# Kernel optimization log

Hardware: AMD Instinct MI355X
Metric: run time of the kernel (lower is better)

Reference implementation:

```python
import jax, jax.numpy as jnp
import numpy as np

B, L, D = 2, 2048, 2560
H, KV, HD = 8, 4, 256
FF = 10240
WINDOW = 1024
ROPE_BASE = 10000.0
EPS = 1e-6


def rmsnorm(x, scale=None):
    x32 = x.astype(jnp.float32)
    var = jnp.mean(jnp.square(x32), axis=-1, keepdims=True)
    xn = x32 * jax.lax.rsqrt(var + EPS)
    return xn if scale is None else xn * scale.astype(jnp.float32)


def apply_rope(x, positions, base):
    # full RoPE (rope_fraction=1.0): rotate pairs (i, i+head_dim//2)
    hd = x.shape[-1]
    half = hd // 2
    timescale = base ** (2.0 * jnp.arange(half, dtype=jnp.float32) / hd)
    ang = positions[:, :, None].astype(jnp.float32) / timescale  # [B,L,half]
    sin = jnp.sin(ang)[:, :, None, :]  # [B,L,1,half]
    cos = jnp.cos(ang)[:, :, None, :]
    x1, x2 = x[..., :half], x[..., half:]
    return jnp.concatenate([x1 * cos - x2 * sin, x2 * cos + x1 * sin], axis=-1)


def setup_inputs() -> dict:
    key = jax.random.key(0)
    ks = jax.random.split(key, 16)
    s = lambda fan_in: 1.0 / np.sqrt(fan_in)
    return {
        "x": jax.random.normal(ks[0], (B, L, D), jnp.float32),
        "positions": jnp.broadcast_to(jnp.arange(L, dtype=jnp.int32), (B, L)),
        "wq": jax.random.normal(ks[1], (D, H * HD), jnp.float32) * s(D),
        "wk": jax.random.normal(ks[2], (D, KV * HD), jnp.float32) * s(D),
        "wv": jax.random.normal(ks[3], (D, KV * HD), jnp.float32) * s(D),
        "wo": jax.random.normal(ks[4], (H * HD, D), jnp.float32) * s(H * HD),
        "q_scale": jnp.ones((HD,), jnp.float32),
        "k_scale": jnp.ones((HD,), jnp.float32),
        "pre_attn_scale": jnp.ones((D,), jnp.float32),
        "post_attn_scale": jnp.ones((D,), jnp.float32),
        "pre_ffw_scale": jnp.ones((D,), jnp.float32),
        "post_ffw_scale": jnp.ones((D,), jnp.float32),
        "w_gate": jax.random.normal(ks[5], (D, FF), jnp.float32) * s(D),
        "w_up": jax.random.normal(ks[6], (D, FF), jnp.float32) * s(D),
        "w_down": jax.random.normal(ks[7], (FF, D), jnp.float32) * s(FF),
    }


def reference(x, positions, wq, wk, wv, wo, q_scale, k_scale,
              pre_attn_scale, post_attn_scale, pre_ffw_scale, post_ffw_scale,
              w_gate, w_up, w_down):
    # --- attention sub-block ---
    h = rmsnorm(x, pre_attn_scale)
    q = (h @ wq).reshape(B, L, H, HD)
    k = (h @ wk).reshape(B, L, KV, HD)
    v = (h @ wv).reshape(B, L, KV, HD)
    q = apply_rope(rmsnorm(q, q_scale), positions, ROPE_BASE)
    k = apply_rope(rmsnorm(k, k_scale), positions, ROPE_BASE)
    v = rmsnorm(v)  # RMSNormNoScale on V
    rep = H // KV
    k = jnp.repeat(k, rep, axis=2)  # [B,L,H,HD]
    v = jnp.repeat(v, rep, axis=2)
    scores = jnp.einsum("bqhd,bkhd->bhqk", q, k)  # NOTE: no 1/sqrt(d) scaling, faithful to source
    i = jnp.arange(L)[:, None]
    j = jnp.arange(L)[None, :]
    mask = (j <= i) & (j > i - WINDOW)  # causal & sliding window
    scores = jnp.where(mask[None, None, :, :], scores, -10000.0)
    probs = jax.nn.softmax(scores.astype(jnp.float32), axis=-1)
    attn = jnp.einsum("bhqk,bkhd->bqhd", probs, v).reshape(B, L, H * HD)
    attn = attn @ wo
    x = x + rmsnorm(attn, post_attn_scale)
    # --- feedforward sub-block (GeGLU) ---
    h = rmsnorm(x, pre_ffw_scale)
    hidden = jax.nn.gelu(h @ w_gate, approximate=False) * (h @ w_up)
    ffw = hidden @ w_down
    x = x + rmsnorm(ffw, post_ffw_scale)
    return x
```

## Files before the change

kernel.cpp:

```cpp
#include <hip/hip_runtime.h>
#include <math.h>

#define DEV __device__ __forceinline__

typedef _Float16 f16;
typedef _Float16 f16x8 __attribute__((ext_vector_type(8)));
typedef _Float16 f16x4 __attribute__((ext_vector_type(4)));
typedef float f32x4 __attribute__((ext_vector_type(4)));

DEV void gload_lds16(const void* g, void* l) {
  __builtin_amdgcn_global_load_lds(
      (const __attribute__((address_space(1))) void*)g,
      (__attribute__((address_space(3))) void*)l, 16, 0, 0);
}

__global__ void transpose_w(const float* __restrict__ src, f16* __restrict__ dst,
                            int R, int C) {
  __shared__ float tile[32][33];
  int c0 = blockIdx.x * 32, r0 = blockIdx.y * 32;
  int tx = threadIdx.x, ty = threadIdx.y;
#pragma unroll
  for (int j = 0; j < 32; j += 8)
    tile[ty + j][tx] = src[(size_t)(r0 + ty + j) * C + c0 + tx];
  __syncthreads();
#pragma unroll
  for (int j = 0; j < 32; j += 8)
    dst[(size_t)(c0 + ty + j) * R + r0 + tx] = (f16)tile[tx][ty + j];
}

__global__ void rope_table_k(float* __restrict__ tab) {
  int idx = blockIdx.x * 256 + threadIdx.x;
  int pos = idx >> 7, j = idx & 127;
  float ts = powf(10000.0f, (float)j * (1.0f / 128.0f));
  float ang = (float)pos / ts;
  tab[pos * 256 + j] = sinf(ang);
  tab[pos * 256 + 128 + j] = cosf(ang);
}

__global__ __launch_bounds__(256) void rmsnorm_f32_f16(
    const float* __restrict__ in, const float* __restrict__ scale,
    f16* __restrict__ out) {
  constexpr int D = 2560, N4 = D / 4;
  const int m = blockIdx.x, tid = threadIdx.x;
  const float* row = in + (size_t)m * D;
  float vals[12];
  float ss = 0.f;
#pragma unroll
  for (int it = 0; it < 3; ++it) {
    int c4 = tid + it * 256;
    if (c4 < N4) {
      float4 v = *(const float4*)(row + c4 * 4);
      vals[it * 4 + 0] = v.x; vals[it * 4 + 1] = v.y;
      vals[it * 4 + 2] = v.z; vals[it * 4 + 3] = v.w;
      ss += v.x * v.x + v.y * v.y + v.z * v.z + v.w * v.w;
    }
  }
#pragma unroll
  for (int off = 32; off; off >>= 1) ss += __shfl_xor(ss, off, 64);
  __shared__ float red[4];
  if ((tid & 63) == 0) red[tid >> 6] = ss;
  __syncthreads();
  float rs = rsqrtf((red[0] + red[1] + red[2] + red[3]) * (1.0f / D) + 1e-6f);
#pragma unroll
  for (int it = 0; it < 3; ++it) {
    int c4 = tid + it * 256;
    if (c4 < N4) {
      float4 sc = *(const float4*)(scale + c4 * 4);
      f16x4 o;
      o[0] = (f16)(vals[it * 4 + 0] * rs * sc.x);
      o[1] = (f16)(vals[it * 4 + 1] * rs * sc.y);
      o[2] = (f16)(vals[it * 4 + 2] * rs * sc.z);
      o[3] = (f16)(vals[it * 4 + 3] * rs * sc.w);
      *(f16x4*)(out + (size_t)m * D + c4 * 4) = o;
    }
  }
}

__global__ __launch_bounds__(256) void residual_rmsnorm(
    const float* x, const f16* __restrict__ y,
    const float* __restrict__ scale, float* out) {
  constexpr int D = 2560, N4 = D / 4;
  const int m = blockIdx.x, tid = threadIdx.x;
  const f16* yr = y + (size_t)m * D;
  float yv[12];
  float ss = 0.f;
#pragma unroll
  for (int it = 0; it < 3; ++it) {
    int c4 = tid + it * 256;
    if (c4 < N4) {
      f16x4 u = *(const f16x4*)(yr + c4 * 4);
      float a = (float)u[0], b = (float)u[1], c = (float)u[2], d = (float)u[3];
      yv[it * 4 + 0] = a; yv[it * 4 + 1] = b; yv[it * 4 + 2] = c; yv[it * 4 + 3] = d;
      ss += a * a + b * b + c * c + d * d;
    }
  }
#pragma unroll
  for (int off = 32; off; off >>= 1) ss += __shfl_xor(ss, off, 64);
  __shared__ float red[4];
  if ((tid & 63) == 0) red[tid >> 6] = ss;
  __syncthreads();
  float rs = rsqrtf((red[0] + red[1] + red[2] + red[3]) * (1.0f / D) + 1e-6f);
#pragma unroll
  for (int it = 0; it < 3; ++it) {
    int c4 = tid + it * 256;
    if (c4 < N4) {
      float4 xv = *(const float4*)(x + (size_t)m * D + c4 * 4);
      float4 sc = *(const float4*)(scale + c4 * 4);
      float4 o;
      o.x = xv.x + yv[it * 4 + 0] * rs * sc.x;
      o.y = xv.y + yv[it * 4 + 1] * rs * sc.y;
      o.z = xv.z + yv[it * 4 + 2] * rs * sc.z;
      o.w = xv.w + yv[it * 4 + 3] * rs * sc.w;
      *(float4*)(out + (size_t)m * D + c4 * 4) = o;
    }
  }
}

__global__ __launch_bounds__(256) void norm_rope_k(
    const f16* __restrict__ qkv, const int* __restrict__ positions,
    const float* __restrict__ q_scale, const float* __restrict__ k_scale,
    const float* __restrict__ tab,
    f16* __restrict__ q_g, f16* __restrict__ k_g, f16* __restrict__ v_n) {
  const int m = blockIdx.x;
  const int tid = threadIdx.x, w = tid >> 6, l = tid & 63;
  const int pos = positions[m];
  const float* srow = tab + (size_t)pos * 256;
  const int c0 = l * 4;
  for (int vi = w; vi < 16; vi += 4) {
    f16x4 u = *(const f16x4*)(qkv + (size_t)m * 4096 + vi * 256 + c0);
    float x0 = (float)u[0], x1 = (float)u[1], x2 = (float)u[2], x3 = (float)u[3];
    float ss = x0 * x0 + x1 * x1 + x2 * x2 + x3 * x3;
#pragma unroll
    for (int off = 32; off; off >>= 1) ss += __shfl_xor(ss, off, 64);
    float rs = rsqrtf(ss * (1.0f / 256.0f) + 1e-6f);
    if (vi < 12) {
      const float* sc = (vi < 8) ? q_scale : k_scale;
      float4 s4 = *(const float4*)(sc + c0);
      float n0 = x0 * rs * s4.x, n1 = x1 * rs * s4.y;
      float n2 = x2 * rs * s4.z, n3 = x3 * rs * s4.w;
      float p0 = __shfl_xor(n0, 32, 64), p1 = __shfl_xor(n1, 32, 64);
      float p2 = __shfl_xor(n2, 32, 64), p3 = __shfl_xor(n3, 32, 64);
      int j0 = c0 & 127;
      float4 sn = *(const float4*)(srow + j0);
      float4 cs = *(const float4*)(srow + 128 + j0);
      float sgn = (l < 32) ? -1.0f : 1.0f;
      f16x4 o;
      o[0] = (f16)(n0 * cs.x + sgn * p0 * sn.x);
      o[1] = (f16)(n1 * cs.y + sgn * p1 * sn.y);
      o[2] = (f16)(n2 * cs.z + sgn * p2 * sn.z);
      o[3] = (f16)(n3 * cs.w + sgn * p3 * sn.w);
      if (vi < 8) *(f16x4*)(q_g + (size_t)m * 2048 + vi * 256 + c0) = o;
      else        *(f16x4*)(k_g + (size_t)m * 1024 + (vi - 8) * 256 + c0) = o;
    } else {
      f16x4 o;
      o[0] = (f16)(x0 * rs); o[1] = (f16)(x1 * rs);
      o[2] = (f16)(x2 * rs); o[3] = (f16)(x3 * rs);
      *(f16x4*)(v_n + (size_t)m * 1024 + (vi - 12) * 256 + c0) = o;
    }
  }
}

__global__ void transpose_v_k(const f16* __restrict__ v_n, f16* __restrict__ vt) {
  __shared__ f16 tile[32][33];
  int bkv = blockIdx.z;
  int b = bkv >> 2, kv = bkv & 3;
  int t0 = blockIdx.x * 32, d0 = blockIdx.y * 32;
  int tx = threadIdx.x, ty = threadIdx.y;
#pragma unroll
  for (int j = 0; j < 32; j += 8)
    tile[ty + j][tx] =
        v_n[(size_t)(b * 2048 + t0 + ty + j) * 1024 + kv * 256 + d0 + tx];
  __syncthreads();
#pragma unroll
  for (int j = 0; j < 32; j += 8)
    vt[((size_t)bkv * 256 + d0 + ty + j) * 2048 + t0 + tx] = tile[tx][ty + j];
}

template <int EPI>
__global__ __launch_bounds__(512, 2) void gemm256(
    const f16* __restrict__ A, const f16* __restrict__ BT,
    f16* __restrict__ C, const f16* __restrict__ aux, int M, int N, int K) {
  extern __shared__ __align__(16) f16 lds[];
  const int tid = threadIdx.x;
  const int w = tid >> 6, l = tid & 63;
  const int l15 = l & 15, lk = l >> 4;
  const int wm = w >> 2, wn = w & 3;

  const int gx = gridDim.x;
  const int nwg = gx * gridDim.y;
  const int orig = blockIdx.y * gx + blockIdx.x;
  const int swz = (orig & 7) * (nwg >> 3) + (orig >> 3);
  const int bn = swz % gx, bm = swz / gx;

  const f16* Ab = A + (size_t)bm * 256 * K;
  const f16* Bb = BT + (size_t)bn * 256 * K;
  const int NT = K >> 6;

  const int srow = tid >> 2;
  const int sg = (tid & 3) ^ ((srow >> 1) & 3);
  const f16* srcA = Ab + (size_t)srow * K + sg * 8;
  const f16* srcB = Bb + (size_t)srow * K + sg * 8;

  auto stage = [&](int op, int kh, int buf, int kt) {
    const f16* src = (op ? srcB : srcA) + kt * 64 + kh * 32;
    f16* dst = lds + ((buf << 2) + (kh << 1) + op) * 8192 + tid * 8;
    gload_lds16(src, dst);
    gload_lds16(src + (size_t)128 * K, dst + 4096);
  };

  const int fcol = (lk ^ ((l15 >> 1) & 3)) << 3;
  const int aoff = (wm * 128 + l15) * 32 + fcol;
  const int boff = 8192 + (wn * 64 + l15) * 32 + fcol;

  f32x4 acc[8][4] = {};

  stage(0, 0, 0, 0);
  stage(1, 0, 0, 0);
  stage(0, 1, 0, 0);
  stage(1, 1, 0, 0);
  if (NT > 1) stage(0, 0, 1, 1);
  asm volatile("s_waitcnt vmcnt(6)" ::: "memory");
  __builtin_amdgcn_s_barrier();
  asm volatile("" ::: "memory");

  for (int t = 0; t < NT; ++t) {
    const int buf = t & 1, nbuf = buf ^ 1;
    const f16* lb0 = lds + buf * 32768;
    const f16* lb1 = lb0 + 16384;
    {
      f16x8 a1[4], b[4], a2[4];
#pragma unroll
      for (int i = 0; i < 4; ++i) a1[i] = *(const f16x8*)(lb0 + aoff + i * 512);
#pragma unroll
      for (int i = 0; i < 4; ++i) b[i] = *(const f16x8*)(lb0 + boff + i * 512);
#pragma unroll
      for (int i = 0; i < 4; ++i) a2[i] = *(const f16x8*)(lb0 + aoff + (4 + i) * 512);
      if (t + 1 < NT) stage(1, 0, nbuf, t + 1);
      __builtin_amdgcn_s_setprio(1);
#pragma unroll
      for (int mi = 0; mi < 4; ++mi)
#pragma unroll
        for (int ni = 0; ni < 4; ++ni)
          acc[mi][ni] = __builtin_amdgcn_mfma_f32_16x16x32_f16(a1[mi], b[ni], acc[mi][ni], 0, 0, 0);
      __builtin_amdgcn_s_setprio(0);
      if (t + 1 < NT) stage(0, 1, nbuf, t + 1);
      __builtin_amdgcn_s_setprio(1);
#pragma unroll
      for (int mi = 0; mi < 4; ++mi)
#pragma unroll
        for (int ni = 0; ni < 4; ++ni)
          acc[4 + mi][ni] = __builtin_amdgcn_mfma_f32_16x16x32_f16(a2[mi], b[ni], acc[4 + mi][ni], 0, 0, 0);
      __builtin_amdgcn_s_setprio(0);
    }
    if (t + 1 < NT) asm volatile("s_waitcnt vmcnt(6)" ::: "memory");
    else            asm volatile("s_waitcnt vmcnt(0)" ::: "memory");
    __builtin_amdgcn_s_barrier();
    asm volatile("" ::: "memory");
    {
      f16x8 a1[4], b[4], a2[4];
#pragma unroll
      for (int i = 0; i < 4; ++i) a1[i] = *(const f16x8*)(lb1 + aoff + i * 512);
#pragma unroll
      for (int i = 0; i < 4; ++i) b[i] = *(const f16x8*)(lb1 + boff + i * 512);
#pragma unroll
      for (int i = 0; i < 4; ++i) a2[i] = *(const f16x8*)(lb1 + aoff + (4 + i) * 512);
      if (t + 1 < NT) stage(1, 1, nbuf, t + 1);
      __builtin_amdgcn_s_setprio(1);
#pragma unroll
      for (int mi = 0; mi < 4; ++mi)
#pragma unroll
        for (int ni = 0; ni < 4; ++ni)
          acc[mi][ni] = __builtin_amdgcn_mfma_f32_16x16x32_f16(a1[mi], b[ni], acc[mi][ni], 0, 0, 0);
      __builtin_amdgcn_s_setprio(0);
      if (t + 2 < NT) stage(0, 0, buf, t + 2);
      __builtin_amdgcn_s_setprio(1);
#pragma unroll
      for (int mi = 0; mi < 4; ++mi)
#pragma unroll
        for (int ni = 0; ni < 4; ++ni)
          acc[4 + mi][ni] = __builtin_amdgcn_mfma_f32_16x16x32_f16(a2[mi], b[ni], acc[4 + mi][ni], 0, 0, 0);
      __builtin_amdgcn_s_setprio(0);
    }
    if (t + 2 < NT)      asm volatile("s_waitcnt vmcnt(6)" ::: "memory");
    else if (t + 1 < NT) asm volatile("s_waitcnt vmcnt(4)" ::: "memory");
    else                 asm volatile("s_waitcnt vmcnt(0)" ::: "memory");
    __builtin_amdgcn_s_barrier();
    asm volatile("" ::: "memory");
  }

#pragma unroll
  for (int mi = 0; mi < 8; ++mi) {
#pragma unroll
    for (int ni = 0; ni < 4; ++ni) {
#pragma unroll
      for (int i = 0; i < 4; ++i) {
        int row = bm * 256 + wm * 128 + mi * 16 + lk * 4 + i;
        int col = bn * 256 + wn * 64 + ni * 16 + l15;
        size_t idx = (size_t)row * N + col;
        float v = acc[mi][ni][i];
        if constexpr (EPI == 1) {
          v = 0.5f * v * (1.0f + erff(v * 0.70710678118654752f));
        } else if constexpr (EPI == 2) {
          v *= (float)aux[idx];
        }
        C[idx] = (f16)v;
      }
    }
  }
}

__global__ __launch_bounds__(256) void flash_attn_k(
    const f16* __restrict__ q_g, const f16* __restrict__ k_g,
    const f16* __restrict__ vt, f16* __restrict__ ctx) {
  constexpr int KP = 264, VP = 40, PP = 40;
  __shared__ f16 Ks[32 * KP];
  __shared__ f16 Vs[256 * VP];
  __shared__ f16 Ps[4][16 * PP];
  const int qt = blockIdx.x, h = blockIdx.y, b = blockIdx.z;
  const int tid = threadIdx.x, w = tid >> 6, l = tid & 63;
  const int l15 = l & 15, lk = l >> 4;
  const int kv = h >> 1;

  f16x8 aq[8];
  const int qrow = qt * 64 + w * 16 + l15;
  const f16* qp = q_g + (size_t)(b * 2048 + qrow) * 2048 + h * 256 + lk * 8;
#pragma unroll
  for (int kc = 0; kc < 8; ++kc) aq[kc] = *(const f16x8*)(qp + kc * 32);

  f32x4 o[16] = {};
  float mrow[4] = {-1e30f, -1e30f, -1e30f, -1e30f};
  float lrow[4] = {0.f, 0.f, 0.f, 0.f};

  int kt_lo = 2 * qt - 32; if (kt_lo < 0) kt_lo = 0;
  const int kt_hi = 2 * qt + 1;
  const int iqb = qt * 64 + w * 16 + lk * 4;

  for (int kt = kt_lo; kt <= kt_hi; ++kt) {
    __syncthreads();
#pragma unroll
    for (int it = 0; it < 4; ++it) {
      int ch = tid + it * 256;
      int jl = ch >> 5, kcc = (ch & 31) * 8;
      *(f16x8*)&Ks[jl * KP + kcc] = *(const f16x8*)(
          k_g + (size_t)(b * 2048 + kt * 32 + jl) * 1024 + kv * 256 + kcc);
      int d = ch >> 2, tc = (ch & 3) * 8;
      *(f16x8*)&Vs[d * VP + tc] = *(const f16x8*)(
          vt + ((size_t)(b * 4 + kv) * 256 + d) * 2048 + kt * 32 + tc);
    }
    __syncthreads();
    f32x4 s[2] = {};
#pragma unroll
    for (int ct = 0; ct < 2; ++ct)
#pragma unroll
      for (int kc = 0; kc < 8; ++kc) {
        f16x8 bk = *(const f16x8*)&Ks[(ct * 16 + l15) * KP + kc * 32 + lk * 8];
        s[ct] = __builtin_amdgcn_mfma_f32_16x16x32_f16(aq[kc], bk, s[ct], 0, 0, 0);
      }
    float pm[4] = {-1e30f, -1e30f, -1e30f, -1e30f};
#pragma unroll
    for (int ct = 0; ct < 2; ++ct)
#pragma unroll
      for (int i = 0; i < 4; ++i) {
        int iq = iqb + i;
        int j = kt * 32 + ct * 16 + l15;
        bool valid = (j <= iq) && (j > iq - 1024);
        float sv = valid ? s[ct][i] : -1e30f;
        s[ct][i] = sv;
        pm[i] = fmaxf(pm[i], sv);
      }
#pragma unroll
    for (int i = 0; i < 4; ++i)
#pragma unroll
      for (int off = 1; off < 16; off <<= 1)
        pm[i] = fmaxf(pm[i], __shfl_xor(pm[i], off, 64));
    float corr[4], rsum[4];
#pragma unroll
    for (int i = 0; i < 4; ++i) {
      float mn = fmaxf(mrow[i], pm[i]);
      corr[i] = __expf(mrow[i] - mn);
      mrow[i] = mn;
      rsum[i] = 0.f;
    }
#pragma unroll
    for (int ct = 0; ct < 2; ++ct)
#pragma unroll
      for (int i = 0; i < 4; ++i) {
        float p = (s[ct][i] > -1e29f) ? __expf(s[ct][i] - mrow[i]) : 0.f;
        s[ct][i] = p;
        rsum[i] += p;
      }
#pragma unroll
    for (int i = 0; i < 4; ++i) {
#pragma unroll
      for (int off = 1; off < 16; off <<= 1) rsum[i] += __shfl_xor(rsum[i], off, 64);
      lrow[i] = lrow[i] * corr[i] + rsum[i];
    }
#pragma unroll
    for (int dt = 0; dt < 16; ++dt)
#pragma unroll
      for (int i = 0; i < 4; ++i) o[dt][i] *= corr[i];
#pragma unroll
    for (int ct = 0; ct < 2; ++ct)
#pragma unroll
      for (int i = 0; i < 4; ++i)
        Ps[w][(lk * 4 + i) * PP + ct * 16 + l15] = (f16)s[ct][i];
    __syncthreads();
    f16x8 pa = *(const f16x8*)&Ps[w][l15 * PP + lk * 8];
#pragma unroll
    for (int dt = 0; dt < 16; ++dt) {
      f16x8 bv = *(const f16x8*)&Vs[(dt * 16 + l15) * VP + lk * 8];
      o[dt] = __builtin_amdgcn_mfma_f32_16x16x32_f16(pa, bv, o[dt], 0, 0, 0);
    }
  }
  float inv[4];
#pragma unroll
  for (int i = 0; i < 4; ++i) inv[i] = 1.0f / lrow[i];
  f16* op = ctx + (size_t)(b * 2048 + qt * 64 + w * 16 + lk * 4) * 2048 + h * 256 + l15;
#pragma unroll
  for (int dt = 0; dt < 16; ++dt)
#pragma unroll
    for (int i = 0; i < 4; ++i)
      op[(size_t)i * 2048 + dt * 16] = (f16)(o[dt][i] * inv[i]);
}

extern "C" void kernel_launch(void* const* d_in, const int* in_sizes, int n_in,
                              void* d_out, int out_size, void* d_ws, size_t ws_size,
                              hipStream_t stream) {
  const float* x = (const float*)d_in[0];
  const int* positions = (const int*)d_in[1];
  const float* wq = (const float*)d_in[2];
  const float* wk = (const float*)d_in[3];
  const float* wv = (const float*)d_in[4];
  const float* wo = (const float*)d_in[5];
  const float* q_scale = (const float*)d_in[6];
  const float* k_scale = (const float*)d_in[7];
  const float* pre_attn = (const float*)d_in[8];
  const float* post_attn = (const float*)d_in[9];
  const float* pre_ffw = (const float*)d_in[10];
  const float* post_ffw = (const float*)d_in[11];
  const float* w_gate = (const float*)d_in[12];
  const float* w_up = (const float*)d_in[13];
  const float* w_down = (const float*)d_in[14];
  float* out = (float*)d_out;

  static bool s_attr = []() {
    hipFuncSetAttribute(reinterpret_cast<const void*>(&gemm256<0>),
                        hipFuncAttributeMaxDynamicSharedMemorySize, 131072);
    hipFuncSetAttribute(reinterpret_cast<const void*>(&gemm256<1>),
                        hipFuncAttributeMaxDynamicSharedMemorySize, 131072);
    hipFuncSetAttribute(reinterpret_cast<const void*>(&gemm256<2>),
                        hipFuncAttributeMaxDynamicSharedMemorySize, 131072);
    return true;
  }();
  (void)s_attr;

  char* ws = (char*)d_ws;
  size_t off = 0;
  auto alloc = [&](size_t bytes) {
    char* p = ws + off;
    off += (bytes + 255) & ~(size_t)255;
    return p;
  };
  f16* wbuf = (f16*)alloc((size_t)10240 * 2560 * 2);
  float* tab = (float*)alloc((size_t)2048 * 256 * 4);
  f16* h     = (f16*)alloc((size_t)4096 * 2560 * 2);
  char* act  = alloc((size_t)92280832);
  f16* qkv    = (f16*)(act);
  f16* q_g    = (f16*)(act + (size_t)33554432);
  f16* k_g    = (f16*)(act + (size_t)33554432 + 16777216);
  f16* v_n    = (f16*)(act + (size_t)33554432 + 16777216 + 8388608);
  f16* vtb    = (f16*)(act + (size_t)33554432 + 16777216 + 2 * 8388608);
  f16* ctx    = (f16*)(act + (size_t)33554432 + 16777216 + 3 * 8388608);
  f16* attn_o = (f16*)(act);
  f16* gbuf = (f16*)(act);
  f16* ffw  = h;
  (void)in_sizes; (void)n_in; (void)out_size; (void)ws_size;

  dim3 tb(32, 8);
  rope_table_k<<<1024, 256, 0, stream>>>(tab);

  rmsnorm_f32_f16<<<4096, 256, 0, stream>>>(x, pre_attn, h);
  transpose_w<<<dim3(2048 / 32, 2560 / 32), tb, 0, stream>>>(wq, wbuf, 2560, 2048);
  transpose_w<<<dim3(1024 / 32, 2560 / 32), tb, 0, stream>>>(wk, wbuf + (size_t)2048 * 2560, 2560, 1024);
  transpose_w<<<dim3(1024 / 32, 2560 / 32), tb, 0, stream>>>(wv, wbuf + (size_t)3072 * 2560, 2560, 1024);
  gemm256<0><<<dim3(4096 / 256, 4096 / 256), 512, 131072, stream>>>(h, wbuf, qkv, nullptr, 4096, 4096, 2560);
  norm_rope_k<<<4096, 256, 0, stream>>>(qkv, positions, q_scale, k_scale, tab, q_g, k_g, v_n);
  transpose_v_k<<<dim3(2048 / 32, 256 / 32, 8), tb, 0, stream>>>(v_n, vtb);
  flash_attn_k<<<dim3(32, 8, 2), 256, 0, stream>>>(q_g, k_g, vtb, ctx);
  transpose_w<<<dim3(2560 / 32, 2048 / 32), tb, 0, stream>>>(wo, wbuf, 2048, 2560);
  gemm256<0><<<dim3(2560 / 256, 4096 / 256), 512, 131072, stream>>>(ctx, wbuf, attn_o, nullptr, 4096, 2560, 2048);
  residual_rmsnorm<<<4096, 256, 0, stream>>>(x, attn_o, post_attn, out);

  rmsnorm_f32_f16<<<4096, 256, 0, stream>>>(out, pre_ffw, h);
  transpose_w<<<dim3(10240 / 32, 2560 / 32), tb, 0, stream>>>(w_gate, wbuf, 2560, 10240);
  gemm256<1><<<dim3(10240 / 256, 4096 / 256), 512, 131072, stream>>>(h, wbuf, gbuf, nullptr, 4096, 10240, 2560);
  transpose_w<<<dim3(10240 / 32, 2560 / 32), tb, 0, stream>>>(w_up, wbuf, 2560, 10240);
  gemm256<2><<<dim3(10240 / 256, 4096 / 256), 512, 131072, stream>>>(h, wbuf, gbuf, gbuf, 4096, 10240, 2560);
  transpose_w<<<dim3(2560 / 32, 10240 / 32), tb, 0, stream>>>(w_down, wbuf, 10240, 2560);
  gemm256<0><<<dim3(2560 / 256, 4096 / 256), 512, 131072, stream>>>(gbuf, wbuf, ffw, nullptr, 4096, 2560, 10240);
  residual_rmsnorm<<<4096, 256, 0, stream>>>(out, ffw, post_ffw, out);
}
```

Measured before the change: 1.209 ms.

## Fuse GeGLU gate and up GEMMs into one kernel with LDS epilogue

Result: slower. 1.259 ms (+4.1%).

```diff
diff --git a/kernel.cpp b/kernel.cpp
--- a/kernel.cpp
+++ b/kernel.cpp
@@ -192,20 +192,34 @@
   const int swz = (orig & 7) * (nwg >> 3) + (orig >> 3);
   const int bn = swz % gx, bm = swz / gx;
 
-  const f16* Ab = A + (size_t)bm * 256 * K;
-  const f16* Bb = BT + (size_t)bn * 256 * K;
   const int NT = K >> 6;
 
   const int srow = tid >> 2;
   const int sg = (tid & 3) ^ ((srow >> 1) & 3);
-  const f16* srcA = Ab + (size_t)srow * K + sg * 8;
-  const f16* srcB = Bb + (size_t)srow * K + sg * 8;
-
-  auto stage = [&](int op, int kh, int buf, int kt) {
-    const f16* src = (op ? srcB : srcA) + kt * 64 + kh * 32;
-    f16* dst = lds + ((buf << 2) + (kh << 1) + op) * 8192 + tid * 8;
-    gload_lds16(src, dst);
-    gload_lds16(src + (size_t)128 * K, dst + 4096);
+  const f16* pA1 = A + (size_t)(bm * 256 + srow) * K + sg * 8;
+  const f16* pA2 = pA1 + (size_t)128 * K;
+  const f16* pB1;
+  const f16* pB2;
+  if constexpr (EPI == 3) {
+    pB1 = BT + (size_t)(bn * 128 + srow) * K + sg * 8;
+    pB2 = aux + (size_t)(bn * 128 + srow) * K + sg * 8;
+  } else {
+    pB1 = BT + (size_t)(bn * 256 + srow) * K + sg * 8;
+    pB2 = pB1 + (size_t)128 * K;
+  }
+
+  auto stage4 = [&](int buf, int kt) {
+    const int kb = kt * 64;
+    f16* base = lds + (buf << 2) * 8192 + tid * 8;
+#pragma unroll
+    for (int kh = 0; kh < 2; ++kh) {
+      f16* dA = base + (kh << 1) * 8192;
+      gload_lds16(pA1 + kb + kh * 32, dA);
+      gload_lds16(pA2 + kb + kh * 32, dA + 4096);
+      f16* dB = base + ((kh << 1) + 1) * 8192;
+      gload_lds16(pB1 + kb + kh * 32, dB);
+      gload_lds16(pB2 + kb + kh * 32, dB + 4096);
+    }
   };
 
   const int fcol = (lk ^ ((l15 >> 1) & 3)) << 3;
@@ -214,96 +228,108 @@
 
   f32x4 acc[8][4] = {};
 
-  stage(0, 0, 0, 0);
-  stage(1, 0, 0, 0);
-  stage(0, 1, 0, 0);
-  stage(1, 1, 0, 0);
-  if (NT > 1) stage(0, 0, 1, 1);
-  asm volatile("s_waitcnt vmcnt(6)" ::: "memory");
+  stage4(0, 0);
+  asm volatile("s_waitcnt vmcnt(0)" ::: "memory");
   __builtin_amdgcn_s_barrier();
   asm volatile("" ::: "memory");
 
   for (int t = 0; t < NT; ++t) {
-    const int buf = t & 1, nbuf = buf ^ 1;
+    const int buf = t & 1;
     const f16* lb0 = lds + buf * 32768;
     const f16* lb1 = lb0 + 16384;
-    {
-      f16x8 a1[4], b[4], a2[4];
-#pragma unroll
-      for (int i = 0; i < 4; ++i) a1[i] = *(const f16x8*)(lb0 + aoff + i * 512);
-#pragma unroll
-      for (int i = 0; i < 4; ++i) b[i] = *(const f16x8*)(lb0 + boff + i * 512);
-#pragma unroll
-      for (int i = 0; i < 4; ++i) a2[i] = *(const f16x8*)(lb0 + aoff + (4 + i) * 512);
-      if (t + 1 < NT) stage(1, 0, nbuf, t + 1);
-      __builtin_amdgcn_s_setprio(1);
-#pragma unroll
-      for (int mi = 0; mi < 4; ++mi)
+    f16x8 a1[4], b1[4], a2[4], a3[4], b2[4], a4[4];
+#pragma unroll
+    for (int i = 0; i < 4; ++i) a1[i] = *(const f16x8*)(lb0 + aoff + i * 512);
+#pragma unroll
+    for (int i = 0; i < 4; ++i) b1[i] = *(const f16x8*)(lb0 + boff + i * 512);
+#pragma unroll
+    for (int i = 0; i < 4; ++i) a2[i] = *(const f16x8*)(lb0 + aoff + (4 + i) * 512);
+    if (t + 1 < NT) stage4(buf ^ 1, t + 1);
+#pragma unroll
+    for (int i = 0; i < 4; ++i) a3[i] = *(const f16x8*)(lb1 + aoff + i * 512);
+#pragma unroll
+    for (int i = 0; i < 4; ++i) b2[i] = *(const f16x8*)(lb1 + boff + i * 512);
+#pragma unroll
+    for (int i = 0; i < 4; ++i) a4[i] = *(const f16x8*)(lb1 + aoff + (4 + i) * 512);
+    __builtin_amdgcn_s_setprio(1);
+#pragma unroll
+    for (int mi = 0; mi < 4; ++mi)
+#pragma unroll
+      for (int ni = 0; ni < 4; ++ni)
+        acc[mi][ni] = __builtin_amdgcn_mfma_f32_16x16x32_f16(a1[mi], b1[ni], acc[mi][ni], 0, 0, 0);
+#pragma unroll
+    for (int mi = 0; mi < 4; ++mi)
+#pragma unroll
+      for (int ni = 0; ni < 4; ++ni)
+        acc[4 + mi][ni] = __builtin_amdgcn_mfma_f32_16x16x32_f16(a2[mi], b1[ni], acc[4 + mi][ni], 0, 0, 0);
+#pragma unroll
+    for (int mi = 0; mi < 4; ++mi)
+#pragma unroll
+      for (int ni = 0; ni < 4; ++ni)
+        acc[mi][ni] = __builtin_amdgcn_mfma_f32_16x16x32_f16(a3[mi], b2[ni], acc[mi][ni], 0, 0, 0);
+#pragma unroll
+    for (int mi = 0; mi < 4; ++mi)
+#pragma unroll
+      for (int ni = 0; ni < 4; ++ni)
+        acc[4 + mi][ni] = __builtin_amdgcn_mfma_f32_16x16x32_f16(a4[mi], b2[ni], acc[4 + mi][ni], 0, 0, 0);
+    __builtin_amdgcn_s_setprio(0);
+    if (t + 1 < NT) {
+      asm volatile("s_waitcnt vmcnt(0)" ::: "memory");
+      __builtin_amdgcn_s_barrier();
+      asm volatile("" ::: "memory");
+    }
+  }
+
+  if constexpr (EPI == 3) {
+    __syncthreads();
+    float* xls = (float*)lds;
+    if (wn < 2) {
+#pragma unroll
+      for (int mi = 0; mi < 8; ++mi)
 #pragma unroll
         for (int ni = 0; ni < 4; ++ni)
-          acc[mi][ni] = __builtin_amdgcn_mfma_f32_16x16x32_f16(a1[mi], b[ni], acc[mi][ni], 0, 0, 0);
-      __builtin_amdgcn_s_setprio(0);
-      if (t + 1 < NT) stage(0, 1, nbuf, t + 1);
-      __builtin_amdgcn_s_setprio(1);
-#pragma unroll
-      for (int mi = 0; mi < 4; ++mi)
+#pragma unroll
+          for (int i = 0; i < 4; ++i) {
+            int row = wm * 128 + mi * 16 + lk * 4 + i;
+            int col = wn * 64 + ni * 16 + l15;
+            float v = acc[mi][ni][i];
+            v = 0.5f * v * (1.0f + erff(v * 0.70710678118654752f));
+            xls[row * 128 + col] = v;
+          }
+    }
+    __syncthreads();
+    if (wn >= 2) {
+#pragma unroll
+      for (int mi = 0; mi < 8; ++mi)
 #pragma unroll
         for (int ni = 0; ni < 4; ++ni)
-          acc[4 + mi][ni] = __builtin_amdgcn_mfma_f32_16x16x32_f16(a2[mi], b[ni], acc[4 + mi][ni], 0, 0, 0);
-      __builtin_amdgcn_s_setprio(0);
-    }
-    if (t + 1 < NT) asm volatile("s_waitcnt vmcnt(6)" ::: "memory");
-    else            asm volatile("s_waitcnt vmcnt(0)" ::: "memory");
-    __builtin_amdgcn_s_barrier();
-    asm volatile("" ::: "memory");
-    {
-      f16x8 a1[4], b[4], a2[4];
-#pragma unroll
-      for (int i = 0; i < 4; ++i) a1[i] = *(const f16x8*)(lb1 + aoff + i * 512);
-#pragma unroll
-      for (int i = 0; i < 4; ++i) b[i] = *(const f16x8*)(lb1 + boff + i * 512);
-#pragma unroll
-      for (int i = 0; i < 4; ++i) a2[i] = *(const f16x8*)(lb1 + aoff + (4 + i) * 512);
-      if (t + 1 < NT) stage(1, 1, nbuf, t + 1);
-      __builtin_amdgcn_s_setprio(1);
-#pragma unroll
-      for (int mi = 0; mi < 4; ++mi)
-#pragma unroll
-        for (int ni = 0; ni < 4; ++ni)
-          acc[mi][ni] = __builtin_amdgcn_mfma_f32_16x16x32_f16(a1[mi], b[ni], acc[mi][ni], 0, 0, 0);
-      __builtin_amdgcn_s_setprio(0);
-      if (t + 2 < NT) stage(0, 0, buf, t + 2);
-      __builtin_amdgcn_s_setprio(1);
-#pragma unroll
-      for (int mi = 0; mi < 4; ++mi)
-#pragma unroll
-        for (int ni = 0; ni < 4; ++ni)
-          acc[4 + mi][ni] = __builtin_amdgcn_mfma_f32_16x16x32_f16(a2[mi], b[ni], acc[4 + mi][ni], 0, 0, 0);
-      __builtin_amdgcn_s_setprio(0);
-    }
-    if (t + 2 < NT)      asm volatile("s_waitcnt vmcnt(6)" ::: "memory");
-    else if (t + 1 < NT) asm volatile("s_waitcnt vmcnt(4)" ::: "memory");
-    else                 asm volatile("s_waitcnt vmcnt(0)" ::: "memory");
-    __builtin_amdgcn_s_barrier();
-    asm volatile("" ::: "memory");
-  }
-
-#pragma unroll
-  for (int mi = 0; mi < 8; ++mi) {
-#pragma unroll
-    for (int ni = 0; ni < 4; ++ni) {
-#pragma unroll
-      for (int i = 0; i < 4; ++i) {
-        int row = bm * 256 + wm * 128 + mi * 16 + lk * 4 + i;
-        int col = bn * 256 + wn * 64 + ni * 16 + l15;
-        size_t idx = (size_t)row * N + col;
-        float v = acc[mi][ni][i];
-        if constexpr (EPI == 1) {
-          v = 0.5f * v * (1.0f + erff(v * 0.70710678118654752f));
-        } else if constexpr (EPI == 2) {
-          v *= (float)aux[idx];
+#pragma unroll
+          for (int i = 0; i < 4; ++i) {
+            int row = wm * 128 + mi * 16 + lk * 4 + i;
+            int colg = (wn - 2) * 64 + ni * 16 + l15;
+            float g = xls[row * 128 + colg];
+            float v = g * acc[mi][ni][i];
+            C[(size_t)(bm * 256 + row) * N + bn * 128 + colg] = (f16)v;
+          }
+    }
+  } else {
+#pragma unroll
+    for (int mi = 0; mi < 8; ++mi) {
+#pragma unroll
+      for (int ni = 0; ni < 4; ++ni) {
+#pragma unroll
+        for (int i = 0; i < 4; ++i) {
+          int row = bm * 256 + wm * 128 + mi * 16 + lk * 4 + i;
+          int col = bn * 256 + wn * 64 + ni * 16 + l15;
+          size_t idx = (size_t)row * N + col;
+          float v = acc[mi][ni][i];
+          if constexpr (EPI == 1) {
+            v = 0.5f * v * (1.0f + erff(v * 0.70710678118654752f));
+          } else if constexpr (EPI == 2) {
+            v *= (float)aux[idx];
+          }
+          C[idx] = (f16)v;
         }
-        C[idx] = (f16)v;
       }
     }
   }
@@ -450,9 +476,19 @@
                         hipFuncAttributeMaxDynamicSharedMemorySize, 131072);
     hipFuncSetAttribute(reinterpret_cast<const void*>(&gemm256<2>),
                         hipFuncAttributeMaxDynamicSharedMemorySize, 131072);
+    hipFuncSetAttribute(reinterpret_cast<const void*>(&gemm256<3>),
+                        hipFuncAttributeMaxDynamicSharedMemorySize, 131072);
     return true;
   }();
   (void)s_attr;
+
+  const size_t WT_BIG   = (size_t)20480 * 2560 * 2;
+  const size_t WT_SMALL = (size_t)10240 * 2560 * 2;
+  const size_t TAB_B = (size_t)2048 * 256 * 4;
+  const size_t H_B   = (size_t)4096 * 2560 * 2;
+  const size_t ACT_B = (size_t)92280832;
+  auto aln = [](size_t v) { return (v + 255) & ~(size_t)255; };
+  const bool big = ws_size >= aln(WT_BIG) + aln(TAB_B) + aln(H_B) + aln(ACT_B);
 
   char* ws = (char*)d_ws;
   size_t off = 0;
@@ -461,10 +497,10 @@
     off += (bytes + 255) & ~(size_t)255;
     return p;
   };
-  f16* wbuf = (f16*)alloc((size_t)10240 * 2560 * 2);
-  float* tab = (float*)alloc((size_t)2048 * 256 * 4);
-  f16* h     = (f16*)alloc((size_t)4096 * 2560 * 2);
-  char* act  = alloc((size_t)92280832);
+  f16* wT    = (f16*)alloc(big ? WT_BIG : WT_SMALL);
+  float* tab = (float*)alloc(TAB_B);
+  f16* h     = (f16*)alloc(H_B);
+  char* act  = alloc(ACT_B);
   f16* qkv    = (f16*)(act);
   f16* q_g    = (f16*)(act + (size_t)33554432);
   f16* k_g    = (f16*)(act + (size_t)33554432 + 16777216);
@@ -474,29 +510,36 @@
   f16* attn_o = (f16*)(act);
   f16* gbuf = (f16*)(act);
   f16* ffw  = h;
-  (void)in_sizes; (void)n_in; (void)out_size; (void)ws_size;
+  f16* wuT  = wT + (size_t)10240 * 2560;
+  (void)in_sizes; (void)n_in; (void)out_size;
 
   dim3 tb(32, 8);
   rope_table_k<<<1024, 256, 0, stream>>>(tab);
 
   rmsnorm_f32_f16<<<4096, 256, 0, stream>>>(x, pre_attn, h);
-  transpose_w<<<dim3(2048 / 32, 2560 / 32), tb, 0, stream>>>(wq, wbuf, 2560, 2048);
-  transpose_w<<<dim3(1024 / 32, 2560 / 32), tb, 0, stream>>>(wk, wbuf + (size_t)2048 * 2560, 2560, 1024);
-  transpose_w<<<dim3(1024 / 32, 2560 / 32), tb, 0, stream>>>(wv, wbuf + (size_t)3072 * 2560, 2560, 1024);
-  gemm256<0><<<dim3(4096 / 256, 4096 / 256), 512, 131072, stream>>>(h, wbuf, qkv, nullptr, 4096, 4096, 2560);
+  transpose_w<<<dim3(2048 / 32, 2560 / 32), tb, 0, stream>>>(wq, wT, 2560, 2048);
+  transpose_w<<<dim3(1024 / 32, 2560 / 32), tb, 0, stream>>>(wk, wT + (size_t)2048 * 2560, 2560, 1024);
+  transpose_w<<<dim3(1024 / 32, 2560 / 32), tb, 0, stream>>>(wv, wT + (size_t)3072 * 2560, 2560, 1024);
+  gemm256<0><<<dim3(4096 / 256, 4096 / 256), 512, 131072, stream>>>(h, wT, qkv, nullptr, 4096, 4096, 2560);
   norm_rope_k<<<4096, 256, 0, stream>>>(qkv, positions, q_scale, k_scale, tab, q_g, k_g, v_n);
   transpose_v_k<<<dim3(2048 / 32, 256 / 32, 8), tb, 0, stream>>>(v_n, vtb);
   flash_attn_k<<<dim3(32, 8, 2), 256, 0, stream>>>(q_g, k_g, vtb, ctx);
-  transpose_w<<<dim3(2560 / 32, 2048 / 32), tb, 0, stream>>>(wo, wbuf, 2048, 2560);
-  gemm256<0><<<dim3(2560 / 256, 4096 / 256), 512, 131072, stream>>>(ctx, wbuf, attn_o, nullptr, 4096, 2560, 2048);
+  transpose_w<<<dim3(2560 / 32, 2048 / 32), tb, 0, stream>>>(wo, wT, 2048, 2560);
+  gemm256<0><<<dim3(2560 / 256, 4096 / 256), 512, 131072, stream>>>(ctx, wT, attn_o, nullptr, 4096, 2560, 2048);
   residual_rmsnorm<<<4096, 256, 0, stream>>>(x, attn_o, post_attn, out);
 
   rmsnorm_f32_f16<<<4096, 256, 0, stream>>>(out, pre_ffw, h);
-  transpose_w<<<dim3(10240 / 32, 2560 / 32), tb, 0, stream>>>(w_gate, wbuf, 2560, 10240);
-  gemm256<1><<<dim3(10240 / 256, 4096 / 256), 512, 131072, stream>>>(h, wbuf, gbuf, nullptr, 4096, 10240, 2560);
-  transpose_w<<<dim3(10240 / 32, 2560 / 32), tb, 0, stream>>>(w_up, wbuf, 2560, 10240);
-  gemm256<2><<<dim3(10240 / 256, 4096 / 256), 512, 131072, stream>>>(h, wbuf, gbuf, gbuf, 4096, 10240, 2560);
-  transpose_w<<<dim3(2560 / 32, 10240 / 32), tb, 0, stream>>>(w_down, wbuf, 10240, 2560);
-  gemm256<0><<<dim3(2560 / 256, 4096 / 256), 512, 131072, stream>>>(gbuf, wbuf, ffw, nullptr, 4096, 2560, 10240);
+  if (big) {
+    transpose_w<<<dim3(10240 / 32, 2560 / 32), tb, 0, stream>>>(w_gate, wT, 2560, 10240);
+    transpose_w<<<dim3(10240 / 32, 2560 / 32), tb, 0, stream>>>(w_up, wuT, 2560, 10240);
+    gemm256<3><<<dim3(80, 16), 512, 131072, stream>>>(h, wT, gbuf, wuT, 4096, 10240, 2560);
+  } else {
+    transpose_w<<<dim3(10240 / 32, 2560 / 32), tb, 0, stream>>>(w_gate, wT, 2560, 10240);
+    gemm256<1><<<dim3(10240 / 256, 4096 / 256), 512, 131072, stream>>>(h, wT, gbuf, nullptr, 4096, 10240, 2560);
+    transpose_w<<<dim3(10240 / 32, 2560 / 32), tb, 0, stream>>>(w_up, wT, 2560, 10240);
+    gemm256<2><<<dim3(10240 / 256, 4096 / 256), 512, 131072, stream>>>(h, wT, gbuf, gbuf, 4096, 10240, 2560);
+  }
+  transpose_w<<<dim3(2560 / 32, 10240 / 32), tb, 0, stream>>>(w_down, wT, 10240, 2560);
+  gemm256<0><<<dim3(2560 / 256, 4096 / 256), 512, 131072, stream>>>(gbuf, wT, ffw, nullptr, 4096, 2560, 10240);
   residual_rmsnorm<<<4096, 256, 0, stream>>>(out, ffw, post_ffw, out);
 }
```
